# Kernel optimization log

Hardware: AMD Instinct MI355X
Metric: run time of the kernel (lower is better)

## Reference

```python
import jax, jax.numpy as jnp
import numpy as np


def setup_inputs() -> dict:
    key = jax.random.key(0)
    k1, k2 = jax.random.split(key)
    B, S = 2048, 512
    # effective pixel intensity samples (positive), per pixel over time
    it_eff = jax.random.uniform(k1, (B, S), minval=0.05, maxval=1.05, dtype=jnp.float32)
    # strictly increasing sample timestamps, dt ~ 1e-4 s
    dts = jax.random.uniform(k2, (B, S), minval=5e-5, maxval=1.5e-4, dtype=jnp.float32)
    ts = jnp.cumsum(dts, axis=1)
    return {
        "it_eff": it_eff,
        "ts": ts,
        # buffer (no softplus): tau_in * it_eff product constant
        "tau_in_it_eff_prod": jnp.float32(1e-4),
        # raw (pre-softplus) learned parameters, softplus(raw) = actual value
        "tau_mil_raw": jnp.float32(-9.0),    # tau_mil_it_eff_prod ~ 1.2e-4
        "A_amp_inv_raw": jnp.float32(-3.0),  # A_amp ~ 20.6
        "A_loop_inv_raw": jnp.float32(-4.0), # A_loop ~ 55
        "tau_out_raw": jnp.float32(-8.0),    # tau_out ~ 3.4e-4 s
        "tau_sf_raw": jnp.float32(-9.0),     # tau_sf ~ 1.2e-4 s
        "tau_diff_raw": jnp.float32(-10.0),  # tau_diff ~ 4.5e-5 s
    }


def _forward(it_eff, ts, tau_in_it_eff_prod, tau_mil_raw, A_amp_inv_raw,
             A_loop_inv_raw, tau_out_raw, tau_sf_raw, tau_diff_raw):
    sp = jax.nn.softplus
    tau_mil_prod = sp(tau_mil_raw)
    A_amp = 1.0 / sp(A_amp_inv_raw)
    A_loop = 1.0 / sp(A_loop_inv_raw)
    tau_out = sp(tau_out_raw)
    omega_c_sf = 1.0 / sp(tau_sf_raw)
    omega_c_diff = 1.0 / sp(tau_diff_raw)

    B, S = it_eff.shape
    K = S - 1
    u = jnp.log(it_eff)                      # effective log-intensity input
    dt = ts[:, 1:] - ts[:, :-1]              # [B, K]

    # Linearize NLTI photoreceptor LPF at steady state = next input sample
    I_ss = it_eff[:, 1:]                     # [B, K]
    tau_in = tau_in_it_eff_prod / I_ss
    tau_mil = tau_mil_prod / I_ss
    denom = (tau_in + tau_mil) * tau_out
    two_zeta_omega_n = (tau_in + tau_out + (A_amp + 1.0) * tau_mil) / denom
    omega_n_sq = (A_loop + 1.0) / denom

    # Augmented matrix for FOH discretization: expm([[A*dt, B*dt, 0],[0,0,1],[0,0,0]])
    # top-left -> Ad, col 4 -> Gamma1, col 5 -> Gamma2 (FOH ramp integral / dt)
    em = jnp.zeros((B, K, 6, 6), dtype=it_eff.dtype)
    em = (em.at[..., 0, 0].set(-two_zeta_omega_n * dt)
            .at[..., 0, 1].set(-omega_n_sq * dt)
            .at[..., 1, 0].set(dt)
            .at[..., 2, 1].set(omega_c_sf * dt)
            .at[..., 2, 2].set(-omega_c_sf * dt)
            .at[..., 3, 2].set(omega_c_diff * dt)
            .at[..., 3, 3].set(-omega_c_diff * dt)
            .at[..., 0, 4].set(omega_n_sq * dt)
            .at[..., 4, 5].set(1.0))
    ms = jax.vmap(jax.scipy.linalg.expm)(em.reshape(-1, 6, 6)).reshape(B, K, 6, 6)
    Ad = ms[..., :4, :4]                     # [B, K, 4, 4]
    G1 = ms[..., :4, 4]                      # [B, K, 4]
    G2 = ms[..., :4, 5]                      # [B, K, 4]
    Bd = G1 - G2                             # coeff of u[k]
    Bt = G2                                  # coeff of u[k+1] (FOH)

    # steady-state initial state at u[0]: x = [0, u0, u0, u0]
    u0 = u[:, 0]
    x0 = jnp.stack([jnp.zeros_like(u0), u0, u0, u0], axis=-1)  # [B, 4]

    def step(x, inp):
        Ad_k, Bd_k, Bt_k, u_k, u_k1 = inp
        x_new = (jnp.einsum('bij,bj->bi', Ad_k, x)
                 + Bd_k * u_k[:, None] + Bt_k * u_k1[:, None])
        return x_new, x_new[:, 3]            # diff-amp LPF output state

    xs = (jnp.moveaxis(Ad, 1, 0), jnp.moveaxis(Bd, 1, 0), jnp.moveaxis(Bt, 1, 0),
          u[:, :-1].T, u[:, 1:].T)
    _, ys = jax.lax.scan(step, x0, xs)       # ys: [K, B]
    y = jnp.concatenate([u0[:, None], ys.T], axis=1)  # [B, S]
    return y


def reference(it_eff, ts, tau_in_it_eff_prod, tau_mil_raw, A_amp_inv_raw,
              A_loop_inv_raw, tau_out_raw, tau_sf_raw, tau_diff_raw):
    return _forward(it_eff, ts, tau_in_it_eff_prod, tau_mil_raw, A_amp_inv_raw,
                    A_loop_inv_raw, tau_out_raw, tau_sf_raw, tau_diff_raw)
```

## Files before the change

### kernel.cpp

```cpp
#include <hip/hip_runtime.h>
#include <math.h>

namespace {
constexpr int BB = 2048;
constexpr int SS = 512;
constexpr int NSQ = 4;
constexpr float SCV = 0.0625f;
}

__device__ __forceinline__ float frcp(float x) { return __builtin_amdgcn_rcpf(x); }
__device__ __forceinline__ float frsq(float x) { return __builtin_amdgcn_rsqf(x); }
__device__ __forceinline__ float flog(float x) {
    return __builtin_amdgcn_logf(x) * 0.69314718056f;
}

struct Aff {
    float a00, a01, a10, a11;
    float a20, a21, a22;
    float a30, a31, a32, a33;
    float c0, c1, c2, c3;
};

__device__ __forceinline__ Aff aff_identity() {
    Aff r;
    r.a00 = 1.f; r.a01 = 0.f; r.a10 = 0.f; r.a11 = 1.f;
    r.a20 = 0.f; r.a21 = 0.f; r.a22 = 1.f;
    r.a30 = 0.f; r.a31 = 0.f; r.a32 = 0.f; r.a33 = 1.f;
    r.c0 = 0.f; r.c1 = 0.f; r.c2 = 0.f; r.c3 = 0.f;
    return r;
}

__device__ __forceinline__ Aff aff_compose(const Aff& s, const Aff& f) {
    Aff r;
    r.a00 = s.a00*f.a00 + s.a01*f.a10;
    r.a01 = s.a00*f.a01 + s.a01*f.a11;
    r.a10 = s.a10*f.a00 + s.a11*f.a10;
    r.a11 = s.a10*f.a01 + s.a11*f.a11;
    r.a20 = s.a20*f.a00 + s.a21*f.a10 + s.a22*f.a20;
    r.a21 = s.a20*f.a01 + s.a21*f.a11 + s.a22*f.a21;
    r.a22 = s.a22*f.a22;
    r.a30 = s.a30*f.a00 + s.a31*f.a10 + s.a32*f.a20 + s.a33*f.a30;
    r.a31 = s.a30*f.a01 + s.a31*f.a11 + s.a32*f.a21 + s.a33*f.a31;
    r.a32 = s.a32*f.a22 + s.a33*f.a32;
    r.a33 = s.a33*f.a33;
    r.c0 = s.a00*f.c0 + s.a01*f.c1 + s.c0;
    r.c1 = s.a10*f.c0 + s.a11*f.c1 + s.c1;
    r.c2 = s.a20*f.c0 + s.a21*f.c1 + s.a22*f.c2 + s.c2;
    r.c3 = s.a30*f.c0 + s.a31*f.c1 + s.a32*f.c2 + s.a33*f.c3 + s.c3;
    return r;
}

__device__ __forceinline__ Aff aff_shfl_up(const Aff& a, int d) {
    Aff r;
    r.a00 = __shfl_up(a.a00, d, 64); r.a01 = __shfl_up(a.a01, d, 64);
    r.a10 = __shfl_up(a.a10, d, 64); r.a11 = __shfl_up(a.a11, d, 64);
    r.a20 = __shfl_up(a.a20, d, 64); r.a21 = __shfl_up(a.a21, d, 64);
    r.a22 = __shfl_up(a.a22, d, 64);
    r.a30 = __shfl_up(a.a30, d, 64); r.a31 = __shfl_up(a.a31, d, 64);
    r.a32 = __shfl_up(a.a32, d, 64); r.a33 = __shfl_up(a.a33, d, 64);
    r.c0 = __shfl_up(a.c0, d, 64); r.c1 = __shfl_up(a.c1, d, 64);
    r.c2 = __shfl_up(a.c2, d, 64); r.c3 = __shfl_up(a.c3, d, 64);
    return r;
}

__device__ __forceinline__ Aff aff_sel_ident(const Aff& p, bool ok) {
    Aff r;
    r.a00 = ok ? p.a00 : 1.f; r.a01 = ok ? p.a01 : 0.f;
    r.a10 = ok ? p.a10 : 0.f; r.a11 = ok ? p.a11 : 1.f;
    r.a20 = ok ? p.a20 : 0.f; r.a21 = ok ? p.a21 : 0.f;
    r.a22 = ok ? p.a22 : 1.f;
    r.a30 = ok ? p.a30 : 0.f; r.a31 = ok ? p.a31 : 0.f;
    r.a32 = ok ? p.a32 : 0.f; r.a33 = ok ? p.a33 : 1.f;
    r.c0 = ok ? p.c0 : 0.f; r.c1 = ok ? p.c1 : 0.f;
    r.c2 = ok ? p.c2 : 0.f; r.c3 = ok ? p.c3 : 0.f;
    return r;
}

__device__ __forceinline__ void aff_apply(const Aff& m, float& x0, float& x1,
                                          float& x2, float& x3) {
    const float y0 = m.a00*x0 + m.a01*x1 + m.c0;
    const float y1 = m.a10*x0 + m.a11*x1 + m.c1;
    const float y2 = m.a20*x0 + m.a21*x1 + m.a22*x2 + m.c2;
    const float y3 = m.a30*x0 + m.a31*x1 + m.a32*x2 + m.a33*x3 + m.c3;
    x0 = y0; x1 = y1; x2 = y2; x3 = y3;
}

__device__ __forceinline__ Aff make_step(
    float Iss, float dt, float uk, float uk1,
    float sprod, float aprod, float tau_out, float Aloop1,
    float wsf, float wdf, float rwsf, float rwdf)
{
    const float rI  = frcp(Iss);
    const float s   = sprod * rI;
    const float idn = frcp(s * tau_out);
    const float a   = fmaf(aprod, rI, tau_out) * idn;
    const float w2  = Aloop1 * idn;
    const float iw  = frsq(w2);
    const float w   = w2 * iw;

    const float dts = dt * SCV;
    const float f00 = -a * dts;
    const float f01 = -w * dts;
    const float f10 =  w * dts;
    const float f21 =  wsf * dts;
    const float f22 = -f21;
    const float f32 =  wdf * dts;
    const float f33 = -f32;

    float t00 = fmaf(f00, 1.0f/6.0f, 1.0f), t01 = f01 * (1.0f/6.0f);
    float t10 = f10 * (1.0f/6.0f),          t11 = 1.0f;
    float c00 = 0.0f, c01 = f21 * (1.0f/6.0f), c10 = 0.0f, c11 = 0.0f;
    float l00 = fmaf(f22, 1.0f/6.0f, 1.0f);
    float l10 = f32 * (1.0f/6.0f);
    float l11 = fmaf(f33, 1.0f/6.0f, 1.0f);
#pragma unroll
    for (int m = 5; m >= 1; --m) {
        const float rm = 1.0f / (float)m;
        const float p00 = f00*t00 + f01*t10;
        const float p01 = f00*t01 + f01*t11;
        const float p10 = f10*t00;
        const float p11 = f10*t01;
        const float q00 = f21*t10 + f22*c00;
        const float q01 = f21*t11 + f22*c01;
        const float q10 = f32*c00 + f33*c10;
        const float q11 = f32*c01 + f33*c11;
        const float m00 = f22*l00;
        const float m10 = f32*l00 + f33*l10;
        const float m11 = f33*l11;
        t00 = fmaf(p00, rm, 1.0f); t01 = p01*rm;
        t10 = p10*rm;              t11 = fmaf(p11, rm, 1.0f);
        c00 = q00*rm; c01 = q01*rm; c10 = q10*rm; c11 = q11*rm;
        l00 = fmaf(m00, rm, 1.0f); l10 = m10*rm; l11 = fmaf(m11, rm, 1.0f);
    }

#pragma unroll
    for (int i = 0; i < NSQ; ++i) {
        const float p00 = t00*t00 + t01*t10;
        const float p01 = t00*t01 + t01*t11;
        const float p10 = t10*t00 + t11*t10;
        const float p11 = t10*t01 + t11*t11;
        const float q00 = c00*t00 + c01*t10 + l00*c00;
        const float q01 = c00*t01 + c01*t11 + l00*c01;
        const float q10 = c10*t00 + c11*t10 + l10*c00 + l11*c10;
        const float q11 = c10*t01 + c11*t11 + l10*c01 + l11*c11;
        const float m00 = l00*l00;
        const float m10 = l10*l00 + l11*l10;
        const float m11 = l11*l11;
        t00 = p00; t01 = p01; t10 = p10; t11 = p11;
        c00 = q00; c01 = q01; c10 = q10; c11 = q11;
        l00 = m00; l10 = m10; l11 = m11;
    }

    const float aw  = a * iw;
    const float rdt = frcp(dt);
    const float rF  = iw * rdt;
    const float rS  = rwsf * rdt;
    const float rD  = rwdf * rdt;
    const float wS  = w * rwsf;
    const float wD  = w * rwdf;
    const float g0u = w * dt;

    const float y0 = t10;
    const float y1 = -fmaf(aw, t10, t00 - 1.0f);
    const float y2 = fmaf(-wS, c00, y1);
    const float y3 = fmaf(-wD, c10, y2);
    const float s0 = y0 - g0u;
    const float z0 = y1 * rF;
    const float z1 = -fmaf(aw, z0, rF * s0);
    const float z2 = fmaf(-y2, rS, z1);
    const float z3 = fmaf(-y3, rD, z2);

    Aff r;
    r.a00 = t00;      r.a01 = w * t01;
    r.a10 = t10 * iw; r.a11 = t11;
    r.a20 = c00 * iw; r.a21 = c01; r.a22 = l00;
    r.a30 = c10 * iw; r.a31 = c11; r.a32 = l10; r.a33 = l11;
    const float G10 = w * y0, G20 = w * z0;
    const float du = uk1 - uk;
    r.c0 = fmaf(G10, uk, G20 * du);
    r.c1 = fmaf(y1,  uk, z1 * du);
    r.c2 = fmaf(y2,  uk, z2 * du);
    r.c3 = fmaf(y3,  uk, z3 * du);
    return r;
}

__global__ __launch_bounds__(256) void pbw_kernel(
    const float* __restrict__ it_eff,
    const float* __restrict__ ts,
    const float* __restrict__ p_tin_prod,
    const float* __restrict__ p_tmil_raw,
    const float* __restrict__ p_aamp_raw,
    const float* __restrict__ p_aloop_raw,
    const float* __restrict__ p_tout_raw,
    const float* __restrict__ p_tsf_raw,
    const float* __restrict__ p_tdiff_raw,
    float* __restrict__ out)
{
    __shared__ float swc[4 * 15];
    __shared__ float sy[SS];

    const int b = blockIdx.x;
    const int t = threadIdx.x;
    const int lane = t & 63;
    const int wv = t >> 6;

    const float tin_prod  = p_tin_prod[0];
    const float tmil_prod = log1pf(expf(p_tmil_raw[0]));
    const float Aamp1     = 1.0f / log1pf(expf(p_aamp_raw[0])) + 1.0f;
    const float Aloop1    = 1.0f / log1pf(expf(p_aloop_raw[0])) + 1.0f;
    const float tau_out   = log1pf(expf(p_tout_raw[0]));
    const float sp_sf     = log1pf(expf(p_tsf_raw[0]));
    const float sp_df     = log1pf(expf(p_tdiff_raw[0]));
    const float wsf       = 1.0f / sp_sf;
    const float wdf       = 1.0f / sp_df;
    const float sprod = tin_prod + tmil_prod;
    const float aprod = fmaf(Aamp1, tmil_prod, tin_prod);

    const float* rowI = it_eff + (size_t)b * SS;
    const float* rowT = ts     + (size_t)b * SS;

    const int k0 = 2 * t;
    const float2 I01 = *(const float2*)(rowI + k0);
    const float2 T01 = *(const float2*)(rowT + k0);
    const bool has2 = (k0 + 2 < SS);
    const float I2 = has2 ? rowI[k0 + 2] : 1.0f;
    const float T2 = has2 ? rowT[k0 + 2] : (T01.y + 1e-4f);
    const float uk0 = flog(I01.x);
    const float uk1 = flog(I01.y);
    const float uk2 = flog(I2);
    const float u0  = flog(rowI[0]);

    Aff m1 = make_step(I01.y, T01.y - T01.x, uk0, uk1,
                       sprod, aprod, tau_out, Aloop1, wsf, wdf, sp_sf, sp_df);
    Aff m2;
    if (has2) {
        m2 = make_step(I2, T2 - T01.y, uk1, uk2,
                       sprod, aprod, tau_out, Aloop1, wsf, wdf, sp_sf, sp_df);
    } else {
        m2 = aff_identity();
    }

    Aff cur = aff_compose(m2, m1);

#pragma unroll
    for (int d = 1; d < 64; d <<= 1) {
        Aff p = aff_shfl_up(cur, d);
        p = aff_sel_ident(p, lane >= d);
        cur = aff_compose(cur, p);
    }

    if (lane == 63) {
        float* dst = &swc[wv * 15];
        dst[0]=cur.a00; dst[1]=cur.a01; dst[2]=cur.a10; dst[3]=cur.a11;
        dst[4]=cur.a20; dst[5]=cur.a21; dst[6]=cur.a22;
        dst[7]=cur.a30; dst[8]=cur.a31; dst[9]=cur.a32; dst[10]=cur.a33;
        dst[11]=cur.c0; dst[12]=cur.c1; dst[13]=cur.c2; dst[14]=cur.c3;
    }
    __syncthreads();

    float x0 = 0.0f, x1 = u0, x2 = u0, x3 = u0;
    for (int j = 0; j < wv; ++j) {
        const float* m = &swc[j * 15];
        Aff wm;
        wm.a00=m[0]; wm.a01=m[1]; wm.a10=m[2]; wm.a11=m[3];
        wm.a20=m[4]; wm.a21=m[5]; wm.a22=m[6];
        wm.a30=m[7]; wm.a31=m[8]; wm.a32=m[9]; wm.a33=m[10];
        wm.c0=m[11]; wm.c1=m[12]; wm.c2=m[13]; wm.c3=m[14];
        aff_apply(wm, x0, x1, x2, x3);
    }

    Aff ex = aff_shfl_up(cur, 1);
    ex = aff_sel_ident(ex, lane >= 1);
    aff_apply(ex, x0, x1, x2, x3);

    aff_apply(m1, x0, x1, x2, x3);
    sy[k0 + 1] = x3;
    if (has2) {
        aff_apply(m2, x0, x1, x2, x3);
        sy[k0 + 2] = x3;
    }
    if (t == 0) sy[0] = u0;

    __syncthreads();

    const int base = b * SS;
    out[base + t]       = sy[t];
    out[base + 256 + t] = sy[256 + t];
}

extern "C" void kernel_launch(void* const* d_in, const int* in_sizes, int n_in,
                              void* d_out, int out_size, void* d_ws, size_t ws_size,
                              hipStream_t stream) {
    const float* it_eff = (const float*)d_in[0];
    const float* ts     = (const float*)d_in[1];
    const float* p2 = (const float*)d_in[2];
    const float* p3 = (const float*)d_in[3];
    const float* p4 = (const float*)d_in[4];
    const float* p5 = (const float*)d_in[5];
    const float* p6 = (const float*)d_in[6];
    const float* p7 = (const float*)d_in[7];
    const float* p8 = (const float*)d_in[8];
    float* out = (float*)d_out;

    pbw_kernel<<<dim3(BB), dim3(256), 0, stream>>>(
        it_eff, ts, p2, p3, p4, p5, p6, p7, p8, out);
}
```

Before: 97.67 us.

## Process four timesteps per thread with 128-thread blocks in affine scan

Each thread now builds four per-step affine maps and composes them locally, so the block uses 128 threads (two wavefronts) instead of 256. The cross-wavefront carry drops to a single stored aggregate, and loads and stores become float4. This cuts the number of shuffle-scan compose rounds per element and the shared-memory carry chain. In exchange each thread does more serial work and holds more registers, and the last thread computes a dummy fourth step that it then discards.

Measured after the change: 91.60 us. 6.2% less time.

```diff
diff --git a/kernel.cpp b/kernel.cpp
--- a/kernel.cpp
+++ b/kernel.cpp
@@ -2,8 +2,9 @@
 #include <math.h>
 
 namespace {
-constexpr int BB = 2048;
-constexpr int SS = 512;
+constexpr int BB  = 2048;
+constexpr int SS  = 512;
+constexpr int TPB = 128;
 constexpr int NSQ = 4;
 constexpr float SCV = 0.0625f;
 }
@@ -184,7 +185,7 @@
     return r;
 }
 
-__global__ __launch_bounds__(256) void pbw_kernel(
+__global__ __launch_bounds__(TPB) void pbw_kernel(
     const float* __restrict__ it_eff,
     const float* __restrict__ ts,
     const float* __restrict__ p_tin_prod,
@@ -196,8 +197,8 @@
     const float* __restrict__ p_tdiff_raw,
     float* __restrict__ out)
 {
-    __shared__ float swc[4 * 15];
-    __shared__ float sy[SS];
+    __shared__ float swc[15];
+    __shared__ float sy[SS + 4];
 
     const int b = blockIdx.x;
     const int t = threadIdx.x;
@@ -219,28 +220,33 @@
     const float* rowI = it_eff + (size_t)b * SS;
     const float* rowT = ts     + (size_t)b * SS;
 
-    const int k0 = 2 * t;
-    const float2 I01 = *(const float2*)(rowI + k0);
-    const float2 T01 = *(const float2*)(rowT + k0);
-    const bool has2 = (k0 + 2 < SS);
-    const float I2 = has2 ? rowI[k0 + 2] : 1.0f;
-    const float T2 = has2 ? rowT[k0 + 2] : (T01.y + 1e-4f);
-    const float uk0 = flog(I01.x);
-    const float uk1 = flog(I01.y);
-    const float uk2 = flog(I2);
+    const int k0 = 4 * t;
+    const float4 I4 = *(const float4*)(rowI + k0);
+    const float4 T4 = *(const float4*)(rowT + k0);
+    const bool last = (t == TPB - 1);
+    const float I_4 = last ? 1.0f : rowI[k0 + 4];
+    const float T_4 = last ? (T4.w + 1e-4f) : rowT[k0 + 4];
+
+    const float u_0 = flog(I4.x);
+    const float u_1 = flog(I4.y);
+    const float u_2 = flog(I4.z);
+    const float u_3 = flog(I4.w);
+    const float u_4 = flog(I_4);
     const float u0  = flog(rowI[0]);
 
-    Aff m1 = make_step(I01.y, T01.y - T01.x, uk0, uk1,
+    Aff m0 = make_step(I4.y, T4.y - T4.x, u_0, u_1,
                        sprod, aprod, tau_out, Aloop1, wsf, wdf, sp_sf, sp_df);
-    Aff m2;
-    if (has2) {
-        m2 = make_step(I2, T2 - T01.y, uk1, uk2,
+    Aff m1 = make_step(I4.z, T4.z - T4.y, u_1, u_2,
                        sprod, aprod, tau_out, Aloop1, wsf, wdf, sp_sf, sp_df);
-    } else {
-        m2 = aff_identity();
-    }
-
-    Aff cur = aff_compose(m2, m1);
+    Aff m2 = make_step(I4.w, T4.w - T4.z, u_2, u_3,
+                       sprod, aprod, tau_out, Aloop1, wsf, wdf, sp_sf, sp_df);
+    Aff m3 = make_step(I_4, T_4 - T4.w, u_3, u_4,
+                       sprod, aprod, tau_out, Aloop1, wsf, wdf, sp_sf, sp_df);
+    if (last) m3 = aff_identity();
+
+    const Aff c01 = aff_compose(m1, m0);
+    const Aff c23 = aff_compose(m3, m2);
+    Aff cur = aff_compose(c23, c01);
 
 #pragma unroll
     for (int d = 1; d < 64; d <<= 1) {
@@ -249,23 +255,21 @@
         cur = aff_compose(cur, p);
     }
 
-    if (lane == 63) {
-        float* dst = &swc[wv * 15];
-        dst[0]=cur.a00; dst[1]=cur.a01; dst[2]=cur.a10; dst[3]=cur.a11;
-        dst[4]=cur.a20; dst[5]=cur.a21; dst[6]=cur.a22;
-        dst[7]=cur.a30; dst[8]=cur.a31; dst[9]=cur.a32; dst[10]=cur.a33;
-        dst[11]=cur.c0; dst[12]=cur.c1; dst[13]=cur.c2; dst[14]=cur.c3;
+    if (wv == 0 && lane == 63) {
+        swc[0]=cur.a00; swc[1]=cur.a01; swc[2]=cur.a10; swc[3]=cur.a11;
+        swc[4]=cur.a20; swc[5]=cur.a21; swc[6]=cur.a22;
+        swc[7]=cur.a30; swc[8]=cur.a31; swc[9]=cur.a32; swc[10]=cur.a33;
+        swc[11]=cur.c0; swc[12]=cur.c1; swc[13]=cur.c2; swc[14]=cur.c3;
     }
     __syncthreads();
 
     float x0 = 0.0f, x1 = u0, x2 = u0, x3 = u0;
-    for (int j = 0; j < wv; ++j) {
-        const float* m = &swc[j * 15];
+    if (wv == 1) {
         Aff wm;
-        wm.a00=m[0]; wm.a01=m[1]; wm.a10=m[2]; wm.a11=m[3];
-        wm.a20=m[4]; wm.a21=m[5]; wm.a22=m[6];
-        wm.a30=m[7]; wm.a31=m[8]; wm.a32=m[9]; wm.a33=m[10];
-        wm.c0=m[11]; wm.c1=m[12]; wm.c2=m[13]; wm.c3=m[14];
+        wm.a00=swc[0]; wm.a01=swc[1]; wm.a10=swc[2]; wm.a11=swc[3];
+        wm.a20=swc[4]; wm.a21=swc[5]; wm.a22=swc[6];
+        wm.a30=swc[7]; wm.a31=swc[8]; wm.a32=swc[9]; wm.a33=swc[10];
+        wm.c0=swc[11]; wm.c1=swc[12]; wm.c2=swc[13]; wm.c3=swc[14];
         aff_apply(wm, x0, x1, x2, x3);
     }
 
@@ -273,19 +277,16 @@
     ex = aff_sel_ident(ex, lane >= 1);
     aff_apply(ex, x0, x1, x2, x3);
 
-    aff_apply(m1, x0, x1, x2, x3);
-    sy[k0 + 1] = x3;
-    if (has2) {
-        aff_apply(m2, x0, x1, x2, x3);
-        sy[k0 + 2] = x3;
-    }
+    aff_apply(m0, x0, x1, x2, x3); sy[k0 + 1] = x3;
+    aff_apply(m1, x0, x1, x2, x3); sy[k0 + 2] = x3;
+    aff_apply(m2, x0, x1, x2, x3); sy[k0 + 3] = x3;
+    aff_apply(m3, x0, x1, x2, x3); sy[k0 + 4] = x3;
     if (t == 0) sy[0] = u0;
 
     __syncthreads();
 
-    const int base = b * SS;
-    out[base + t]       = sy[t];
-    out[base + 256 + t] = sy[256 + t];
+    float4* po = (float4*)(out + (size_t)b * SS);
+    po[t] = *(const float4*)&sy[4 * t];
 }
 
 extern "C" void kernel_launch(void* const* d_in, const int* in_sizes, int n_in,
@@ -302,6 +303,6 @@
     const float* p8 = (const float*)d_in[8];
     float* out = (float*)d_out;
 
-    pbw_kernel<<<dim3(BB), dim3(256), 0, stream>>>(
+    pbw_kernel<<<dim3(BB), dim3(TPB), 0, stream>>>(
         it_eff, ts, p2, p3, p4, p5, p6, p7, p8, out);
 }
```
